# Kernel tuning notes

Hardware: AMD Instinct MI355X
Metric: run time of the kernel (lower is better)

Reference implementation:

```python
import jax, jax.numpy as jnp
import numpy as np
from jax import lax

LEAK = 0.2
GN_EPS = 1e-5
K_NEIGH = 16
GROUPS = 4


def knn_idx(coor_k, coor_q, k):
    # coor_k: [B,Nk,3], coor_q: [B,Nq,3] -> [B,Nq,k] indices of k nearest in coor_k
    d = (jnp.sum(coor_q * coor_q, -1, keepdims=True)
         - 2.0 * jnp.einsum('bqc,bkc->bqk', coor_q, coor_k)
         + jnp.sum(coor_k * coor_k, -1)[:, None, :])
    _, idx = lax.top_k(-d, k)
    return idx


def graph_feature(coor_q, x_q, coor_k, x_k, k):
    # coor_*: [B,3,N*]; x_q: [B,C,Nq]; x_k: [B,C,Nk] -> [B,2C,Nq,k]
    idx = knn_idx(lax.stop_gradient(coor_k).transpose(0, 2, 1),
                  lax.stop_gradient(coor_q).transpose(0, 2, 1), k)
    B = x_k.shape[0]
    x_k_t = x_k.transpose(0, 2, 1)                      # [B,Nk,C]
    b_idx = jnp.arange(B)[:, None, None]
    nb = x_k_t[b_idx, idx]                              # [B,Nq,k,C]
    nb = nb.transpose(0, 3, 1, 2)                       # [B,C,Nq,k]
    xq = x_q[:, :, :, None]                             # [B,C,Nq,1]
    return jnp.concatenate([nb - xq, jnp.broadcast_to(xq, nb.shape)], axis=1)


def conv_gn_lrelu_max(f, w, gamma, beta):
    # f: [B,Cin,N,k]; w: [Cout,Cin] -> [B,Cout,N] (max over k)
    y = jnp.einsum('oc,bcnk->bonk', w, f)
    B, C, N, Kk = y.shape
    g = y.reshape(B, GROUPS, C // GROUPS, N, Kk)
    mu = g.mean((2, 3, 4), keepdims=True)
    var = g.var((2, 3, 4), keepdims=True)
    g = (g - mu) * lax.rsqrt(var + GN_EPS)
    y = g.reshape(B, C, N, Kk) * gamma[None, :, None, None] + beta[None, :, None, None]
    y = jnp.where(y >= 0, y, LEAK * y)
    return y.max(axis=-1)


def fps(xyz, n):
    # xyz: [B,N,3] -> [B,n] int32 (furthest point sampling, start at index 0)
    B, N, _ = xyz.shape
    d0 = jnp.sum((xyz - xyz[:, :1]) ** 2, -1)           # dist to point 0
    def body(dist, _):
        idx = jnp.argmax(dist, -1)                       # [B]
        nxt = jnp.take_along_axis(xyz, idx[:, None, None], 1)
        dist = jnp.minimum(dist, jnp.sum((xyz - nxt) ** 2, -1))
        return dist, idx
    _, idxs = lax.scan(body, d0, None, length=n - 1)     # [n-1,B]
    first = jnp.zeros((1, B), idxs.dtype)
    return jnp.concatenate([first, idxs], 0).T           # [B,n]


def fps_downsample(coor, x, n):
    # coor: [B,3,N], x: [B,C,N] -> ([B,3,n], [B,C,n])
    idx = fps(lax.stop_gradient(coor).transpose(0, 2, 1), n)
    comb = jnp.concatenate([coor, x], axis=1)            # [B,3+C,N]
    b_idx = jnp.arange(coor.shape[0])[:, None]
    new = comb.transpose(0, 2, 1)[b_idx, idx].transpose(0, 2, 1)
    return new[:, :3], new[:, 3:]


def setup_inputs() -> dict:
    key = jax.random.key(0)
    ks = jax.random.split(key, 16)
    s = 0.1
    return {
        'x': jax.random.normal(ks[0], (32, 2048, 3), jnp.float32),
        'w_in': jax.random.normal(ks[1], (8, 3), jnp.float32) * s,
        'b_in': jnp.zeros((8,), jnp.float32),
        'w1': jax.random.normal(ks[2], (32, 16), jnp.float32) * s,
        'g1': jnp.ones((32,), jnp.float32), 'be1': jnp.zeros((32,), jnp.float32),
        'w2': jax.random.normal(ks[3], (64, 64), jnp.float32) * s,
        'g2': jnp.ones((64,), jnp.float32), 'be2': jnp.zeros((64,), jnp.float32),
        'w3': jax.random.normal(ks[4], (64, 128), jnp.float32) * s,
        'g3': jnp.ones((64,), jnp.float32), 'be3': jnp.zeros((64,), jnp.float32),
        'w4': jax.random.normal(ks[5], (256, 128), jnp.float32) * s,
        'g4': jnp.ones((256,), jnp.float32), 'be4': jnp.zeros((256,), jnp.float32),
        'num0': 512,
        'num1': 128,
    }


def reference(x, w_in, b_in, w1, g1, be1, w2, g2, be2, w3, g3, be3, w4, g4, be4, num0, num1):
    coor = x.transpose(0, 2, 1)                          # [B,3,N]
    f = jnp.einsum('oc,bcn->bon', w_in, coor) + b_in[None, :, None]  # input_trans
    f = graph_feature(coor, f, coor, f, K_NEIGH)         # [B,16,N,k]
    f = conv_gn_lrelu_max(f, w1, g1, be1)                # [B,32,N]
    coor_q, f_q = fps_downsample(coor, f, num0)
    f = graph_feature(coor_q, f_q, coor, f, K_NEIGH)     # [B,64,num0,k]
    f = conv_gn_lrelu_max(f, w2, g2, be2)                # [B,64,num0]
    coor = coor_q
    f = graph_feature(coor, f, coor, f, K_NEIGH)         # [B,128,num0,k]
    f = conv_gn_lrelu_max(f, w3, g3, be3)                # [B,64,num0]
    coor_q, f_q = fps_downsample(coor, f, num1)
    f = graph_feature(coor_q, f_q, coor, f, K_NEIGH)     # [B,128,num1,k]
    f = conv_gn_lrelu_max(f, w4, g4, be4)                # [B,256,num1]
    coor = coor_q
    return coor.transpose(0, 2, 1), f.transpose(0, 2, 1)  # [B,num1,3], [B,num1,256]
```

## Files before the change

kernel.cpp:

```cpp
#include <hip/hip_runtime.h>

#define BB 32
#define NPTS0 2048
#define KNB 16
#define KC 256

constexpr int ilog2c(int n){ int l=0; while(n>1){ n>>=1; ++l; } return l; }

static __device__ __forceinline__ float sq3(float a, float b, float c){
  return __fadd_rn(__fadd_rn(__fmul_rn(a,a),__fmul_rn(b,b)),__fmul_rn(c,c));
}

template<int CTRL, int RM>
static __device__ __forceinline__ float dpp_maxf(float v){
  int s = __builtin_amdgcn_update_dpp(__float_as_int(v), __float_as_int(v), CTRL, RM, 0xF, false);
  return fmaxf(v, __int_as_float(s));
}
template<int CTRL, int RM>
static __device__ __forceinline__ unsigned dpp_minu(unsigned v){
  unsigned s = (unsigned)__builtin_amdgcn_update_dpp((int)v, (int)v, CTRL, RM, 0xF, false);
  return s < v ? s : v;
}

static __device__ __forceinline__ void proj_body(const float* __restrict__ x,
    const float* __restrict__ w, const float* __restrict__ bias, float* __restrict__ f0,
    int blk)
{
  int gid = blk*256 + threadIdx.x;
  if (gid >= BB*NPTS0) return;
  float x0 = x[gid*3+0], x1 = x[gid*3+1], x2 = x[gid*3+2];
  #pragma unroll
  for (int o = 0; o < 8; ++o){
    float acc = __fmul_rn(w[o*3+0], x0);
    acc = __fmaf_rn(w[o*3+1], x1, acc);
    acc = __fmaf_rn(w[o*3+2], x2, acc);
    f0[gid*8+o] = __fadd_rn(acc, bias[o]);
  }
}

#define KDECL(I) float th##I = __builtin_inff(); int ti##I = 0;
#define KINS(I,J) if (th##I < th##J){ float tv=th##I; th##I=th##J; th##J=tv; \
                                      int tj=ti##I; ti##I=ti##J; ti##J=tj; }
#define KST(I) pd[base+I] = th##I; pi[base+I] = (unsigned char)ti##I;

static __device__ __forceinline__ void knn_part_body(const float* __restrict__ qpts,
    const float* __restrict__ kpts, int Nq, int Nk, int nkc,
    float* __restrict__ pd, unsigned char* __restrict__ pi,
    int b, int qcb, int kc, float4* kk4)
{
  int tid = threadIdx.x;
  {
    int j = kc*KC + tid;
    float a = kpts[(b*Nk+j)*3+0];
    float c = kpts[(b*Nk+j)*3+1];
    float d = kpts[(b*Nk+j)*3+2];
    kk4[tid] = make_float4(a, c, d, sq3(a,c,d));
  }
  __syncthreads();
  int q = qcb*256 + tid;
  if (q >= Nq) return;
  float qx = qpts[(b*Nq+q)*3+0], qy = qpts[(b*Nq+q)*3+1], qz = qpts[(b*Nq+q)*3+2];
  float qq = sq3(qx,qy,qz);
  KDECL(0) KDECL(1) KDECL(2) KDECL(3) KDECL(4) KDECL(5) KDECL(6) KDECL(7)
  KDECL(8) KDECL(9) KDECL(10) KDECL(11) KDECL(12) KDECL(13) KDECL(14) KDECL(15)
  for (int j=0;j<KC;j++){
    float4 k4 = kk4[j];
    float dot = __fmul_rn(qx,k4.x);
    dot = __fmaf_rn(qy,k4.y,dot);
    dot = __fmaf_rn(qz,k4.z,dot);
    float d = __fadd_rn(__fsub_rn(qq, __fmul_rn(2.0f,dot)), k4.w);
    if (d < th15){
      th15 = d; ti15 = j;
      KINS(15,14) KINS(14,13) KINS(13,12) KINS(12,11) KINS(11,10) KINS(10,9)
      KINS(9,8) KINS(8,7) KINS(7,6) KINS(6,5) KINS(5,4) KINS(4,3) KINS(3,2)
      KINS(2,1) KINS(1,0)
    }
  }
  size_t base = ((size_t)(b*Nq+q)*nkc + kc)*KNB;
  KST(0) KST(1) KST(2) KST(3) KST(4) KST(5) KST(6) KST(7)
  KST(8) KST(9) KST(10) KST(11) KST(12) KST(13) KST(14) KST(15)
}

#define FPS_LOAD(T) float px##T, py##T, pz##T, d##T; { int i_=T*256+tid; \
  px##T=P[i_*3+0]; py##T=P[i_*3+1]; pz##T=P[i_*3+2]; \
  float dx_=__fsub_rn(px##T,c0x), dy_=__fsub_rn(py##T,c0y), dz_=__fsub_rn(pz##T,c0z); \
  d##T=sq3(dx_,dy_,dz_); bm=fmaxf(bm,d##T); }
#define FPS_MATCH(T) if (d##T == m_w) ci = (unsigned)(T*256 + tid);
#define FPS_OWN(T) if ((idx_w>>8) == T##u){ cx=px##T; cy=py##T; cz=pz##T; }
#define FPS_UPD(T) { float dx_=__fsub_rn(px##T,sx), dy_=__fsub_rn(py##T,sy), dz_=__fsub_rn(pz##T,sz); \
  float nd_=sq3(dx_,dy_,dz_); d##T=fminf(d##T,nd_); nbm=fmaxf(nbm,d##T); }

#define FPS_REDUCE_AND_PICK \
    float v = bm; \
    v = dpp_maxf<0x111, 0xF>(v); \
    v = dpp_maxf<0x112, 0xF>(v); \
    v = dpp_maxf<0x114, 0xF>(v); \
    v = dpp_maxf<0x118, 0xF>(v); \
    v = dpp_maxf<0x142, 0xA>(v); \
    v = dpp_maxf<0x143, 0xC>(v); \
    float m_w = __int_as_float(__builtin_amdgcn_readlane(__float_as_int(v), 63)); \
    unsigned ci = 0xFFFFFFFFu;

#define FPS_MIN_AND_MERGE \
    ci = dpp_minu<0x111, 0xF>(ci); \
    ci = dpp_minu<0x112, 0xF>(ci); \
    ci = dpp_minu<0x114, 0xF>(ci); \
    ci = dpp_minu<0x118, 0xF>(ci); \
    ci = dpp_minu<0x142, 0xA>(ci); \
    ci = dpp_minu<0x143, 0xC>(ci); \
    unsigned idx_w = (unsigned)__builtin_amdgcn_readlane((int)ci, 63); \
    int par = s & 1;

#define FPS_CROSSWAVE \
    __syncthreads(); \
    float4 q0 = *(const float4*)&swp[par][0][0]; float z0 = swp[par][0][4]; \
    float4 q1 = *(const float4*)&swp[par][1][0]; float z1 = swp[par][1][4]; \
    float4 q2 = *(const float4*)&swp[par][2][0]; float z2 = swp[par][2][4]; \
    float4 q3 = *(const float4*)&swp[par][3][0]; float z3 = swp[par][3][4]; \
    float mm = q0.x; unsigned mi = __float_as_uint(q0.y); \
    float sx = q0.z, sy = q0.w, sz = z0; \
    if (q1.x > mm || (q1.x == mm && __float_as_uint(q1.y) < mi)){ \
      mm = q1.x; mi = __float_as_uint(q1.y); sx = q1.z; sy = q1.w; sz = z1; } \
    if (q2.x > mm || (q2.x == mm && __float_as_uint(q2.y) < mi)){ \
      mm = q2.x; mi = __float_as_uint(q2.y); sx = q2.z; sy = q2.w; sz = z2; } \
    if (q3.x > mm || (q3.x == mm && __float_as_uint(q3.y) < mi)){ \
      mm = q3.x; mi = __float_as_uint(q3.y); sx = q3.z; sy = q3.w; sz = z3; } \
    if (tid == 0) oidx[b*S+s] = (int)mi;

static __device__ __forceinline__ void fps8_body(const float* __restrict__ pts,
    int S, int* __restrict__ oidx, int b, float* swpraw)
{
  float (*swp)[4][8] = reinterpret_cast<float(*)[4][8]>(swpraw);
  int tid = threadIdx.x, wid = tid >> 6;
  const float* P = pts + (size_t)b*2048*3;
  float c0x = P[0], c0y = P[1], c0z = P[2];
  float bm = -1.0f;
  FPS_LOAD(0) FPS_LOAD(1) FPS_LOAD(2) FPS_LOAD(3)
  FPS_LOAD(4) FPS_LOAD(5) FPS_LOAD(6) FPS_LOAD(7)
  if (tid == 0) oidx[b*S+0] = 0;
  for (int s=1; s<S; ++s){
    FPS_REDUCE_AND_PICK
    FPS_MATCH(7) FPS_MATCH(6) FPS_MATCH(5) FPS_MATCH(4)
    FPS_MATCH(3) FPS_MATCH(2) FPS_MATCH(1) FPS_MATCH(0)
    FPS_MIN_AND_MERGE
    if (tid == (int)(idx_w & 255u)){
      float cx = px0, cy = py0, cz = pz0;
      FPS_OWN(1) FPS_OWN(2) FPS_OWN(3) FPS_OWN(4) FPS_OWN(5) FPS_OWN(6) FPS_OWN(7)
      float4* wp = (float4*)&swp[par][wid][0];
      *wp = make_float4(m_w, __uint_as_float(idx_w), cx, cy);
      swp[par][wid][4] = cz;
    }
    FPS_CROSSWAVE
    float nbm = -1.0f;
    FPS_UPD(0) FPS_UPD(1) FPS_UPD(2) FPS_UPD(3)
    FPS_UPD(4) FPS_UPD(5) FPS_UPD(6) FPS_UPD(7)
    bm = nbm;
  }
}

static __device__ __forceinline__ void fps2_body(const float* __restrict__ pts,
    int S, int* __restrict__ oidx, int b, float* swpraw)
{
  float (*swp)[4][8] = reinterpret_cast<float(*)[4][8]>(swpraw);
  int tid = threadIdx.x, wid = tid >> 6;
  const float* P = pts + (size_t)b*512*3;
  float c0x = P[0], c0y = P[1], c0z = P[2];
  float bm = -1.0f;
  FPS_LOAD(0) FPS_LOAD(1)
  if (tid == 0) oidx[b*S+0] = 0;
  for (int s=1; s<S; ++s){
    FPS_REDUCE_AND_PICK
    FPS_MATCH(1) FPS_MATCH(0)
    FPS_MIN_AND_MERGE
    if (tid == (int)(idx_w & 255u)){
      float cx = px0, cy = py0, cz = pz0;
      FPS_OWN(1)
      float4* wp = (float4*)&swp[par][wid][0];
      *wp = make_float4(m_w, __uint_as_float(idx_w), cx, cy);
      swp[par][wid][4] = cz;
    }
    FPS_CROSSWAVE
    float nbm = -1.0f;
    FPS_UPD(0) FPS_UPD(1)
    bm = nbm;
  }
}

__global__ __launch_bounds__(256) void fused1_kernel(const float* __restrict__ x,
    const float* __restrict__ w_in, const float* __restrict__ b_in,
    float* __restrict__ f0, float* __restrict__ pd1, unsigned char* __restrict__ pi1,
    int* __restrict__ fidx0)
{
  __shared__ __align__(16) char sm[4096];
  int bid = blockIdx.x;
  if (bid < 32){
    __builtin_amdgcn_s_setprio(3);
    fps8_body(x, 512, fidx0, bid, (float*)sm);
  } else if (bid < 32+2048){
    int r = bid - 32;
    int b = r & 31; int rest = r >> 5;
    knn_part_body(x, x, 2048, 2048, 8, pd1, pi1, b, rest & 7, rest >> 3, (float4*)sm);
  } else {
    proj_body(x, w_in, b_in, f0, bid - 2080);
  }
}

__global__ __launch_bounds__(256) void fused2_kernel(const float* __restrict__ coorq1,
    const float* __restrict__ x,
    float* __restrict__ pd2, unsigned char* __restrict__ pi2,
    float* __restrict__ pd3, unsigned char* __restrict__ pi3,
    int* __restrict__ fidx1)
{
  __shared__ __align__(16) char sm[4096];
  int bid = blockIdx.x;
  if (bid < 32){
    __builtin_amdgcn_s_setprio(3);
    fps2_body(coorq1, 128, fidx1, bid, (float*)sm);
  } else if (bid < 32+512){
    int r = bid - 32;
    int b = r & 31; int rest = r >> 5;
    knn_part_body(coorq1, x, 512, 2048, 8, pd2, pi2, b, rest & 1, rest >> 1, (float4*)sm);
  } else {
    int r = bid - 544;
    int b = r & 31; int rest = r >> 5;
    knn_part_body(coorq1, coorq1, 512, 512, 2, pd3, pi3, b, rest & 1, rest >> 1, (float4*)sm);
  }
}

__global__ __launch_bounds__(256) void knn_part_kernel(const float* __restrict__ qpts,
    const float* __restrict__ kpts, int Nq, int Nk,
    float* __restrict__ pd, unsigned char* __restrict__ pi)
{
  __shared__ __align__(16) float4 kk4[KC];
  knn_part_body(qpts, kpts, Nq, Nk, gridDim.z, pd, pi,
                blockIdx.x, blockIdx.y, blockIdx.z, kk4);
}

__global__ __launch_bounds__(256) void knn_merge_kernel(const float* __restrict__ pd,
    const unsigned char* __restrict__ pi, int Nq, int nkc, int* __restrict__ oidx)
{
  int gid = blockIdx.x*256 + threadIdx.x;
  if (gid >= BB*Nq) return;
  float th[KNB]; int ti[KNB];
  #pragma unroll
  for (int i=0;i<KNB;i++){ th[i] = __builtin_inff(); ti[i] = 0; }
  size_t base = (size_t)gid*nkc*KNB;
  for (int kc=0;kc<nkc;kc++){
    size_t cb = base + (size_t)kc*KNB;
    for (int i=0;i<KNB;i++){
      float d = pd[cb+i];
      if (d >= th[KNB-1]) break;
      int j = kc*KC + (int)pi[cb+i];
      th[KNB-1] = d; ti[KNB-1] = j;
      #pragma unroll
      for (int m=KNB-1;m>0;--m){
        if (th[m] < th[m-1]){
          float tv=th[m]; th[m]=th[m-1]; th[m-1]=tv;
          int tj=ti[m]; ti[m]=ti[m-1]; ti[m-1]=tj;
        }
      }
    }
  }
  #pragma unroll
  for (int i=0;i<KNB;i++) oidx[gid*KNB + i] = ti[i];
}

template<int C, int O, bool DIFF>
__global__ __launch_bounds__(256) void gemv_kernel(const float* __restrict__ fin,
    const float* __restrict__ W, float* __restrict__ out, int Npts)
{
  constexpr int NT = O/8;
  constexpr int LNT = ilog2c(NT);
  int gid = blockIdx.x*256 + threadIdx.x;
  if (gid >= BB*Npts*NT) return;
  int tile = gid & (NT-1);
  int pn = gid >> LNT;
  const float* frow = fin + pn*C;
  float f[C];
  #pragma unroll
  for (int c=0;c<C;c++) f[c] = frow[c];
  float acc[8];
  const float* wbase = W + (tile*8)*(2*C);
  #pragma unroll
  for (int oo=0;oo<8;oo++){
    const float* wrow = wbase + oo*(2*C);
    float a = 0.f;
    #pragma unroll
    for (int c=0;c<C;c++){
      float wv = DIFF ? __fsub_rn(wrow[C+c], wrow[c]) : wrow[c];
      a = __fmaf_rn(wv, f[c], a);
    }
    acc[oo] = a;
  }
  float* orow = out + pn*O + tile*8;
  #pragma unroll
  for (int oo=0;oo<8;oo++) orow[oo] = acc[oo];
}

template<int O>
__global__ __launch_bounds__(256) void stats_kernel(const float* __restrict__ A,
    const float* __restrict__ Bq, const int* __restrict__ idx, int Nq, int Nk,
    double* __restrict__ part)
{
  constexpr int O4 = O/4;
  constexpr int LO4 = ilog2c(O4);
  int b = blockIdx.x, g = blockIdx.y, split = blockIdx.z;
  int nsplit = gridDim.z;
  int qlen = Nq / nsplit;
  int q0 = split * qlen;
  int tid = threadIdx.x;
  int total = qlen * KNB * O4;
  double s1 = 0.0, s2 = 0.0;
  for (int s = tid; s < total; s += 256){
    int oin = s & (O4-1);
    int rest = s >> LO4;
    int kk = rest & (KNB-1);
    int q = q0 + (rest >> 4);
    int j = idx[(b*Nq+q)*KNB + kk];
    float y = A[(b*Nk+j)*O + g*O4 + oin] + Bq[(b*Nq+q)*O + g*O4 + oin];
    s1 += (double)y;
    s2 += (double)y * (double)y;
  }
  #pragma unroll
  for (int m=32;m>0;m>>=1){ s1 += __shfl_down(s1,m); s2 += __shfl_down(s2,m); }
  __shared__ double sh1[4], sh2[4];
  int lane = tid & 63, w = tid >> 6;
  if (lane == 0){ sh1[w]=s1; sh2[w]=s2; }
  __syncthreads();
  if (tid == 0){
    double t1 = (sh1[0]+sh1[1])+(sh1[2]+sh1[3]);
    double t2 = (sh2[0]+sh2[1])+(sh2[2]+sh2[3]);
    int pi = (b*4+g)*nsplit + split;
    part[pi*2] = t1; part[pi*2+1] = t2;
  }
}

__global__ __launch_bounds__(128) void statsred_kernel(const double* __restrict__ part,
    int nsplit, double cnt, float* __restrict__ stats)
{
  int t = threadIdx.x;
  if (t >= BB*4) return;
  double s1=0.0, s2=0.0;
  for (int i=0;i<nsplit;i++){ s1 += part[(t*nsplit+i)*2]; s2 += part[(t*nsplit+i)*2+1]; }
  double mean = s1/cnt;
  double var = s2/cnt - mean*mean;
  double rstd = 1.0 / sqrt(var + 1e-5);
  stats[t*2] = (float)mean;
  stats[t*2+1] = (float)rstd;
}

template<int O>
__global__ __launch_bounds__(256) void final_kernel(const float* __restrict__ A,
    const float* __restrict__ Bq, const int* __restrict__ idx,
    const float* __restrict__ stats, const float* __restrict__ gamma,
    const float* __restrict__ beta, float* __restrict__ fout, int Nq, int Nk)
{
  constexpr int LO = ilog2c(O);
  constexpr int LO4 = ilog2c(O/4);
  int b = blockIdx.y;
  int t = blockIdx.x*256 + threadIdx.x;
  if (t >= Nq*O) return;
  int o = t & (O-1);
  int q = t >> LO;
  int g = o >> LO4;
  float mu   = stats[(b*4+g)*2];
  float rstd = stats[(b*4+g)*2+1];
  float gam = gamma[o], bet = beta[o];
  float bq = Bq[(b*Nq+q)*O + o];
  const int* ip = idx + (b*Nq+q)*KNB;
  float m = -__builtin_inff();
  #pragma unroll
  for (int kk=0;kk<KNB;kk++){
    int j = ip[kk];
    float y = A[(b*Nk+j)*O + o] + bq;
    float yn = __fmul_rn(__fsub_rn(y, mu), rstd);
    float yv = __fadd_rn(__fmul_rn(yn, gam), bet);
    float l = yv >= 0.f ? yv : 0.2f*yv;
    m = fmaxf(m, l);
  }
  fout[(b*Nq+q)*O + o] = m;
}

template<int C>
__global__ __launch_bounds__(256) void gather_kernel(const int* __restrict__ fidx,
    const float* __restrict__ pts, const float* __restrict__ fin,
    float* __restrict__ cq, float* __restrict__ fq, int Nin, int Nout)
{
  int gid = blockIdx.x*256 + threadIdx.x;
  if (gid >= BB*Nout) return;
  int b = gid / Nout;
  int i = gid - b*Nout;
  int src = fidx[b*Nout + i];
  #pragma unroll
  for (int c=0;c<3;c++) cq[gid*3+c] = pts[(b*Nin+src)*3+c];
  #pragma unroll
  for (int c=0;c<C;c++) fq[gid*C+c] = fin[(b*Nin+src)*C+c];
}

__global__ __launch_bounds__(256) void gatherc_kernel(const int* __restrict__ fidx,
    const float* __restrict__ pts, float* __restrict__ cq, int Nin, int Nout)
{
  int gid = blockIdx.x*256 + threadIdx.x;
  if (gid >= BB*Nout) return;
  int b = gid / Nout;
  int i = gid - b*Nout;
  int src = fidx[b*Nout + i];
  #pragma unroll
  for (int c=0;c<3;c++) cq[gid*3+c] = pts[(b*Nin+src)*3+c];
}

template<int C>
__global__ __launch_bounds__(256) void gatherf_kernel(const int* __restrict__ fidx,
    const float* __restrict__ fin, float* __restrict__ fq, int Nin, int Nout)
{
  int gid = blockIdx.x*256 + threadIdx.x;
  if (gid >= BB*Nout) return;
  int b = gid / Nout;
  int i = gid - b*Nout;
  int src = fidx[b*Nout + i];
  #pragma unroll
  for (int c=0;c<C;c++) fq[gid*C+c] = fin[(b*Nin+src)*C+c];
}

extern "C" void kernel_launch(void* const* d_in, const int* in_sizes, int n_in,
                              void* d_out, int out_size, void* d_ws, size_t ws_size,
                              hipStream_t stream)
{
  (void)in_sizes; (void)n_in; (void)out_size; (void)ws_size;
  const float* x    = (const float*)d_in[0];
  const float* w_in = (const float*)d_in[1];
  const float* b_in = (const float*)d_in[2];
  const float* w1 = (const float*)d_in[3];
  const float* g1 = (const float*)d_in[4];
  const float* be1= (const float*)d_in[5];
  const float* w2 = (const float*)d_in[6];
  const float* g2 = (const float*)d_in[7];
  const float* be2= (const float*)d_in[8];
  const float* w3 = (const float*)d_in[9];
  const float* g3 = (const float*)d_in[10];
  const float* be3= (const float*)d_in[11];
  const float* w4 = (const float*)d_in[12];
  const float* g4 = (const float*)d_in[13];
  const float* be4= (const float*)d_in[14];

  float* out = (float*)d_out;
  float* coor_out = out;
  float* f_out = out + BB*128*3;

  char* ws = (char*)d_ws;
  size_t off = 0;
  auto alloc = [&](size_t bytes)->void*{ void* p = ws + off; off += (bytes + 255) & ~(size_t)255; return p; };

  float* f0     = (float*)alloc((size_t)BB*2048*8*4);
  int*   idx1   = (int*)  alloc((size_t)BB*2048*16*4);
  float* f1     = (float*)alloc((size_t)BB*2048*32*4);
  double* part  = (double*)alloc((size_t)BB*4*8*2*8);
  float* statsv = (float*)alloc((size_t)BB*4*2*4);
  int*   fidx0  = (int*)  alloc((size_t)BB*512*4);
  float* coorq1 = (float*)alloc((size_t)BB*512*3*4);
  float* fq1    = (float*)alloc((size_t)BB*512*32*4);
  int*   idx2   = (int*)  alloc((size_t)BB*512*16*4);
  float* f2     = (float*)alloc((size_t)BB*512*64*4);
  int*   idx3   = (int*)  alloc((size_t)BB*512*16*4);
  float* f3     = (float*)alloc((size_t)BB*512*64*4);
  int*   fidx1  = (int*)  alloc((size_t)BB*128*4);
  float* fq2    = (float*)alloc((size_t)BB*128*64*4);
  int*   idx4   = (int*)  alloc((size_t)BB*128*16*4);
  float* pd2          = (float*)alloc((size_t)BB*512*8*KNB*4);
  unsigned char* pi2  = (unsigned char*)alloc((size_t)BB*512*8*KNB);
  float* pd3          = (float*)alloc((size_t)BB*512*2*KNB*4);
  unsigned char* pi3  = (unsigned char*)alloc((size_t)BB*512*2*KNB);
  float* pd4          = (float*)alloc((size_t)BB*128*2*KNB*4);
  unsigned char* pi4  = (unsigned char*)alloc((size_t)BB*128*2*KNB);

  char* U = (char*)alloc((size_t)48<<20);
  float* pd1         = (float*)U;
  unsigned char* pi1 = (unsigned char*)(U + ((size_t)34<<20));
  float* A  = (float*)U;
  float* Bq = (float*)(U + ((size_t)20<<20));

  auto cdiv = [](int a, int b){ return (a+b-1)/b; };

  fused1_kernel<<<2336,256,0,stream>>>(x, w_in, b_in, f0, pd1, pi1, fidx0);

  knn_merge_kernel<<<cdiv(BB*2048,256),256,0,stream>>>(pd1, pi1, 2048, 8, idx1);
  gemv_kernel<8,32,false><<<cdiv(BB*2048*4,256),256,0,stream>>>(f0, w1, A, 2048);
  gemv_kernel<8,32,true ><<<cdiv(BB*2048*4,256),256,0,stream>>>(f0, w1, Bq, 2048);
  stats_kernel<32><<<dim3(BB,4,8),256,0,stream>>>(A, Bq, idx1, 2048, 2048, part);
  statsred_kernel<<<1,128,0,stream>>>(part, 8, 8.0*2048*16, statsv);
  final_kernel<32><<<dim3(cdiv(2048*32,256),BB),256,0,stream>>>(A, Bq, idx1, statsv, g1, be1, f1, 2048, 2048);

  gather_kernel<32><<<cdiv(BB*512,256),256,0,stream>>>(fidx0, x, f1, coorq1, fq1, 2048, 512);

  fused2_kernel<<<672,256,0,stream>>>(coorq1, x, pd2, pi2, pd3, pi3, fidx1);

  knn_merge_kernel<<<cdiv(BB*512,256),256,0,stream>>>(pd2, pi2, 512, 8, idx2);
  knn_merge_kernel<<<cdiv(BB*512,256),256,0,stream>>>(pd3, pi3, 512, 2, idx3);

  gatherc_kernel<<<cdiv(BB*128,256),256,0,stream>>>(fidx1, coorq1, coor_out, 512, 128);
  knn_part_kernel<<<dim3(BB,1,2),256,0,stream>>>(coor_out, coorq1, 128, 512, pd4, pi4);
  knn_merge_kernel<<<cdiv(BB*128,256),256,0,stream>>>(pd4, pi4, 128, 2, idx4);

  gemv_kernel<32,64,false><<<cdiv(BB*2048*8,256),256,0,stream>>>(f1, w2, A, 2048);
  gemv_kernel<32,64,true ><<<cdiv(BB*512*8,256),256,0,stream>>>(fq1, w2, Bq, 512);
  stats_kernel<64><<<dim3(BB,4,8),256,0,stream>>>(A, Bq, idx2, 512, 2048, part);
  statsred_kernel<<<1,128,0,stream>>>(part, 8, 16.0*512*16, statsv);
  final_kernel<64><<<dim3(cdiv(512*64,256),BB),256,0,stream>>>(A, Bq, idx2, statsv, g2, be2, f2, 512, 2048);

  gemv_kernel<64,64,false><<<cdiv(BB*512*8,256),256,0,stream>>>(f2, w3, A, 512);
  gemv_kernel<64,64,true ><<<cdiv(BB*512*8,256),256,0,stream>>>(f2, w3, Bq, 512);
  stats_kernel<64><<<dim3(BB,4,8),256,0,stream>>>(A, Bq, idx3, 512, 512, part);
  statsred_kernel<<<1,128,0,stream>>>(part, 8, 16.0*512*16, statsv);
  final_kernel<64><<<dim3(cdiv(512*64,256),BB),256,0,stream>>>(A, Bq, idx3, statsv, g3, be3, f3, 512, 512);

  gatherf_kernel<64><<<cdiv(BB*128,256),256,0,stream>>>(fidx1, f3, fq2, 512, 128);
  gemv_kernel<64,256,false><<<cdiv(BB*512*32,256),256,0,stream>>>(f3, w4, A, 512);
  gemv_kernel<64,256,true ><<<cdiv(BB*128*32,256),256,0,stream>>>(fq2, w4, Bq, 128);
  stats_kernel<256><<<dim3(BB,4,8),256,0,stream>>>(A, Bq, idx4, 128, 512, part);
  statsred_kernel<<<1,128,0,stream>>>(part, 8, 64.0*128*16, statsv);
  final_kernel<256><<<dim3(cdiv(128*256,256),BB),256,0,stream>>>(A, Bq, idx4, statsv, g4, be4, f_out, 128, 512);
}
```

Before: 1.439 ms.

## Restructure GroupNorm stats to one thread per neighbor pair and buffer FPS indices in LDS

The GroupNorm statistics kernel is rewritten so each thread handles one (query, neighbor) pair. It reads full A and Bq rows with float4 loads and accumulates all four groups, partly in float before promoting to double, which replaces per-element double accumulation and the separate per-group grid dimension. The FPS loops now store chosen indices in shared memory and write them to global memory once after the loop, taking global stores off the serial critical path. The float partial sums slightly change rounding, and the grid drops to 256 blocks, which may lower parallelism for the stats pass.

```diff
diff --git a/kernel.cpp b/kernel.cpp
--- a/kernel.cpp
+++ b/kernel.cpp
@@ -125,19 +125,20 @@
       mm = q2.x; mi = __float_as_uint(q2.y); sx = q2.z; sy = q2.w; sz = z2; } \
     if (q3.x > mm || (q3.x == mm && __float_as_uint(q3.y) < mi)){ \
       mm = q3.x; mi = __float_as_uint(q3.y); sx = q3.z; sy = q3.w; sz = z3; } \
-    if (tid == 0) oidx[b*S+s] = (int)mi;
+    if (tid == 0) oibuf[s] = (int)mi;
 
 static __device__ __forceinline__ void fps8_body(const float* __restrict__ pts,
-    int S, int* __restrict__ oidx, int b, float* swpraw)
-{
-  float (*swp)[4][8] = reinterpret_cast<float(*)[4][8]>(swpraw);
+    int S, int* __restrict__ oidx, int b, char* smraw)
+{
+  float (*swp)[4][8] = reinterpret_cast<float(*)[4][8]>(smraw);
+  int* oibuf = reinterpret_cast<int*>(smraw + 256);
   int tid = threadIdx.x, wid = tid >> 6;
   const float* P = pts + (size_t)b*2048*3;
   float c0x = P[0], c0y = P[1], c0z = P[2];
   float bm = -1.0f;
   FPS_LOAD(0) FPS_LOAD(1) FPS_LOAD(2) FPS_LOAD(3)
   FPS_LOAD(4) FPS_LOAD(5) FPS_LOAD(6) FPS_LOAD(7)
-  if (tid == 0) oidx[b*S+0] = 0;
+  if (tid == 0) oibuf[0] = 0;
   for (int s=1; s<S; ++s){
     FPS_REDUCE_AND_PICK
     FPS_MATCH(7) FPS_MATCH(6) FPS_MATCH(5) FPS_MATCH(4)
@@ -156,18 +157,21 @@
     FPS_UPD(4) FPS_UPD(5) FPS_UPD(6) FPS_UPD(7)
     bm = nbm;
   }
+  __syncthreads();
+  for (int s2 = tid; s2 < S; s2 += 256) oidx[b*S + s2] = oibuf[s2];
 }
 
 static __device__ __forceinline__ void fps2_body(const float* __restrict__ pts,
-    int S, int* __restrict__ oidx, int b, float* swpraw)
-{
-  float (*swp)[4][8] = reinterpret_cast<float(*)[4][8]>(swpraw);
+    int S, int* __restrict__ oidx, int b, char* smraw)
+{
+  float (*swp)[4][8] = reinterpret_cast<float(*)[4][8]>(smraw);
+  int* oibuf = reinterpret_cast<int*>(smraw + 256);
   int tid = threadIdx.x, wid = tid >> 6;
   const float* P = pts + (size_t)b*512*3;
   float c0x = P[0], c0y = P[1], c0z = P[2];
   float bm = -1.0f;
   FPS_LOAD(0) FPS_LOAD(1)
-  if (tid == 0) oidx[b*S+0] = 0;
+  if (tid == 0) oibuf[0] = 0;
   for (int s=1; s<S; ++s){
     FPS_REDUCE_AND_PICK
     FPS_MATCH(1) FPS_MATCH(0)
@@ -184,6 +188,8 @@
     FPS_UPD(0) FPS_UPD(1)
     bm = nbm;
   }
+  __syncthreads();
+  for (int s2 = tid; s2 < S; s2 += 256) oidx[b*S + s2] = oibuf[s2];
 }
 
 __global__ __launch_bounds__(256) void fused1_kernel(const float* __restrict__ x,
@@ -195,7 +201,7 @@
   int bid = blockIdx.x;
   if (bid < 32){
     __builtin_amdgcn_s_setprio(3);
-    fps8_body(x, 512, fidx0, bid, (float*)sm);
+    fps8_body(x, 512, fidx0, bid, sm);
   } else if (bid < 32+2048){
     int r = bid - 32;
     int b = r & 31; int rest = r >> 5;
@@ -215,7 +221,7 @@
   int bid = blockIdx.x;
   if (bid < 32){
     __builtin_amdgcn_s_setprio(3);
-    fps2_body(coorq1, 128, fidx1, bid, (float*)sm);
+    fps2_body(coorq1, 128, fidx1, bid, sm);
   } else if (bid < 32+512){
     int r = bid - 32;
     int b = r & 31; int rest = r >> 5;
@@ -298,40 +304,62 @@
 }
 
 template<int O>
-__global__ __launch_bounds__(256) void stats_kernel(const float* __restrict__ A,
+__global__ __launch_bounds__(256) void stats2_kernel(const float* __restrict__ A,
     const float* __restrict__ Bq, const int* __restrict__ idx, int Nq, int Nk,
     double* __restrict__ part)
 {
   constexpr int O4 = O/4;
-  constexpr int LO4 = ilog2c(O4);
-  int b = blockIdx.x, g = blockIdx.y, split = blockIdx.z;
-  int nsplit = gridDim.z;
-  int qlen = Nq / nsplit;
-  int q0 = split * qlen;
+  int b = blockIdx.x, split = blockIdx.y, nsplit = gridDim.y;
+  int qlen = Nq / nsplit, q0 = split*qlen;
   int tid = threadIdx.x;
-  int total = qlen * KNB * O4;
-  double s1 = 0.0, s2 = 0.0;
-  for (int s = tid; s < total; s += 256){
-    int oin = s & (O4-1);
-    int rest = s >> LO4;
-    int kk = rest & (KNB-1);
-    int q = q0 + (rest >> 4);
+  int pairs = qlen * KNB;
+  double s1[4] = {0.0,0.0,0.0,0.0};
+  double s2[4] = {0.0,0.0,0.0,0.0};
+  for (int p = tid; p < pairs; p += 256){
+    int q = q0 + (p >> 4);
+    int kk = p & 15;
     int j = idx[(b*Nq+q)*KNB + kk];
-    float y = A[(b*Nk+j)*O + g*O4 + oin] + Bq[(b*Nq+q)*O + g*O4 + oin];
-    s1 += (double)y;
-    s2 += (double)y * (double)y;
-  }
-  #pragma unroll
-  for (int m=32;m>0;m>>=1){ s1 += __shfl_down(s1,m); s2 += __shfl_down(s2,m); }
-  __shared__ double sh1[4], sh2[4];
+    const float* arow = A + (size_t)(b*Nk+j)*O;
+    const float* brow = Bq + (size_t)(b*Nq+q)*O;
+    #pragma unroll
+    for (int g=0; g<4; ++g){
+      float cs1 = 0.f, cs2 = 0.f;
+      #pragma unroll
+      for (int c=0; c<O4; c+=4){
+        float4 a4 = *(const float4*)(arow + g*O4 + c);
+        float4 b4 = *(const float4*)(brow + g*O4 + c);
+        float y0 = a4.x+b4.x, y1 = a4.y+b4.y, y2 = a4.z+b4.z, y3 = a4.w+b4.w;
+        cs1 += ((y0+y1)+(y2+y3));
+        cs2 = fmaf(y0,y0,cs2); cs2 = fmaf(y1,y1,cs2);
+        cs2 = fmaf(y2,y2,cs2); cs2 = fmaf(y3,y3,cs2);
+      }
+      s1[g] += (double)cs1;
+      s2[g] += (double)cs2;
+    }
+  }
+  #pragma unroll
+  for (int m=32;m>0;m>>=1){
+    #pragma unroll
+    for (int g=0; g<4; ++g){
+      s1[g] += __shfl_down(s1[g], m);
+      s2[g] += __shfl_down(s2[g], m);
+    }
+  }
+  __shared__ double sh[4][8];
   int lane = tid & 63, w = tid >> 6;
-  if (lane == 0){ sh1[w]=s1; sh2[w]=s2; }
+  if (lane == 0){
+    #pragma unroll
+    for (int g=0; g<4; ++g){ sh[w][g*2] = s1[g]; sh[w][g*2+1] = s2[g]; }
+  }
   __syncthreads();
   if (tid == 0){
-    double t1 = (sh1[0]+sh1[1])+(sh1[2]+sh1[3]);
-    double t2 = (sh2[0]+sh2[1])+(sh2[2]+sh2[3]);
-    int pi = (b*4+g)*nsplit + split;
-    part[pi*2] = t1; part[pi*2+1] = t2;
+    #pragma unroll
+    for (int g=0; g<4; ++g){
+      double t1 = (sh[0][g*2]+sh[1][g*2]) + (sh[2][g*2]+sh[3][g*2]);
+      double t2 = (sh[0][g*2+1]+sh[1][g*2+1]) + (sh[2][g*2+1]+sh[3][g*2+1]);
+      int pi = (b*4+g)*nsplit + split;
+      part[pi*2] = t1; part[pi*2+1] = t2;
+    }
   }
 }
 
@@ -486,7 +514,7 @@
   knn_merge_kernel<<<cdiv(BB*2048,256),256,0,stream>>>(pd1, pi1, 2048, 8, idx1);
   gemv_kernel<8,32,false><<<cdiv(BB*2048*4,256),256,0,stream>>>(f0, w1, A, 2048);
   gemv_kernel<8,32,true ><<<cdiv(BB*2048*4,256),256,0,stream>>>(f0, w1, Bq, 2048);
-  stats_kernel<32><<<dim3(BB,4,8),256,0,stream>>>(A, Bq, idx1, 2048, 2048, part);
+  stats2_kernel<32><<<dim3(BB,8),256,0,stream>>>(A, Bq, idx1, 2048, 2048, part);
   statsred_kernel<<<1,128,0,stream>>>(part, 8, 8.0*2048*16, statsv);
   final_kernel<32><<<dim3(cdiv(2048*32,256),BB),256,0,stream>>>(A, Bq, idx1, statsv, g1, be1, f1, 2048, 2048);
 
@@ -503,20 +531,20 @@
 
   gemv_kernel<32,64,false><<<cdiv(BB*2048*8,256),256,0,stream>>>(f1, w2, A, 2048);
   gemv_kernel<32,64,true ><<<cdiv(BB*512*8,256),256,0,stream>>>(fq1, w2, Bq, 512);
-  stats_kernel<64><<<dim3(BB,4,8),256,0,stream>>>(A, Bq, idx2, 512, 2048, part);
+  stats2_kernel<64><<<dim3(BB,8),256,0,stream>>>(A, Bq, idx2, 512, 2048, part);
   statsred_kernel<<<1,128,0,stream>>>(part, 8, 16.0*512*16, statsv);
   final_kernel<64><<<dim3(cdiv(512*64,256),BB),256,0,stream>>>(A, Bq, idx2, statsv, g2, be2, f2, 512, 2048);
 
   gemv_kernel<64,64,false><<<cdiv(BB*512*8,256),256,0,stream>>>(f2, w3, A, 512);
   gemv_kernel<64,64,true ><<<cdiv(BB*512*8,256),256,0,stream>>>(f2, w3, Bq, 512);
-  stats_kernel<64><<<dim3(BB,4,8),256,0,stream>>>(A, Bq, idx3, 512, 512, part);
+  stats2_kernel<64><<<dim3(BB,8),256,0,stream>>>(A, Bq, idx3, 512, 512, part);
   statsred_kernel<<<1,128,0,stream>>>(part, 8, 16.0*512*16, statsv);
   final_kernel<64><<<dim3(cdiv(512*64,256),BB),256,0,stream>>>(A, Bq, idx3, statsv, g3, be3, f3, 512, 512);
 
   gatherf_kernel<64><<<cdiv(BB*128,256),256,0,stream>>>(fidx1, f3, fq2, 512, 128);
   gemv_kernel<64,256,false><<<cdiv(BB*512*32,256),256,0,stream>>>(f3, w4, A, 512);
   gemv_kernel<64,256,true ><<<cdiv(BB*128*32,256),256,0,stream>>>(fq2, w4, Bq, 128);
-  stats_kernel<256><<<dim3(BB,4,8),256,0,stream>>>(A, Bq, idx4, 128, 512, part);
+  stats2_kernel<256><<<dim3(BB,8),256,0,stream>>>(A, Bq, idx4, 128, 512, part);
   statsred_kernel<<<1,128,0,stream>>>(part, 8, 64.0*128*16, statsv);
   final_kernel<256><<<dim3(cdiv(128*256,256),BB),256,0,stream>>>(A, Bq, idx4, statsv, g4, be4, f_out, 128, 512);
 }
```

Result: faster. 1.364 ms (-5.2%).
